# Optimization experiments

Measured on AMD Instinct MI355X. Metric: run time of the kernel, lower is better.

The kernel has to match this reference:

```python
import jax, jax.numpy as jnp
import numpy as np

B, N, DIM, H, DH = 2, 2048, 512, 8, 64
EPS = 1e-3  # eps added after relu feature map, per original


def setup_inputs() -> dict:
    key = jax.random.key(0)
    k0, k1, k2, k3, k4 = jax.random.split(key, 5)
    s_in = 1.0 / np.sqrt(DIM)
    s_out = 1.0 / np.sqrt(H * DH)
    return {
        "x": jax.random.normal(k0, (B, N, DIM), jnp.float32),
        "Wq": jax.random.normal(k1, (DIM, H * DH), jnp.float32) * s_in,
        "Wk": jax.random.normal(k2, (DIM, H * DH), jnp.float32) * s_in,
        "Wv": jax.random.normal(k3, (DIM, H * DH), jnp.float32) * s_in,
        "Wo": jax.random.normal(k4, (H * DH, DIM), jnp.float32) * s_out,
        "bo": jnp.zeros((DIM,), jnp.float32),
    }


def causal_linear_attn(q, k, v, eps=EPS):
    # bucket_size == 1 path of the original causal_linear_attn (blindspot_size=1):
    # relu feature map + eps, running cumsums of k and of the outer product k v^T.
    q = jax.nn.relu(q) + eps
    k = jax.nn.relu(k) + eps
    k_cum = jnp.cumsum(k, axis=2)                                  # [b,h,n,d]
    ctx = jnp.cumsum(k[..., :, None] * v[..., None, :], axis=2)    # [b,h,n,d,e]
    d_inv = 1.0 / jnp.einsum('bhnd,bhnd->bhn', q, k_cum)           # [b,h,n]
    return jnp.einsum('bhnd,bhnde,bhn->bhne', q, ctx, d_inv)       # [b,h,n,e]


def reference(x, Wq, Wk, Wv, Wo, bo):
    b, n, _ = x.shape
    split = lambda t: t.reshape(b, n, H, DH).transpose(0, 2, 1, 3)  # [b,h,n,dh]
    q = split(x @ Wq)
    k = split(x @ Wk)
    v = split(x @ Wv)
    out = causal_linear_attn(q, k, v)
    out = out.transpose(0, 2, 1, 3).reshape(b, n, H * DH)
    return out @ Wo + bo
```

## Files before the change

### kernel.cpp

```cpp
#include <hip/hip_runtime.h>

constexpr int kB   = 2;
constexpr int kN   = 2048;
constexpr int kDIM = 512;
constexpr int kH   = 8;
constexpr int kDH  = 64;
constexpr int kBH  = kB * kH;
constexpr int NROWS = kB * kN;
constexpr int CHUNK = 64;
constexpr int NCH   = kN / CHUNK;
constexpr int CBSTRIDE = kDH * kDH + kDH;
constexpr float kEPS = 1e-3f;

typedef _Float16 f16x8 __attribute__((ext_vector_type(8)));
typedef _Float16 f16x4 __attribute__((ext_vector_type(4)));
typedef float    floatx4 __attribute__((ext_vector_type(4)));

__device__ __forceinline__ void async_copy16(void* lds, const void* g) {
    __builtin_amdgcn_global_load_lds(
        (const __attribute__((address_space(1))) void*)g,
        (__attribute__((address_space(3))) void*)lds,
        16, 0, 0);
}

__global__ __launch_bounds__(256)
void prep_kernel(const float* __restrict__ Wq, const float* __restrict__ Wk,
                 const float* __restrict__ Wv, const float* __restrict__ Wo,
                 _Float16* __restrict__ WT, _Float16* __restrict__ WoT)
{
    __shared__ float tile[32][33];
    const int z = blockIdx.z;
    const float* src = (z == 0) ? Wq : (z == 1) ? Wk : (z == 2) ? Wv : Wo;
    _Float16* dst = (z < 3) ? (WT + (size_t)z * 512 * 512) : WoT;
    const int r0 = blockIdx.y * 32, c0 = blockIdx.x * 32;
    const int tr = threadIdx.x >> 5, tc = threadIdx.x & 31;
    #pragma unroll
    for (int i = 0; i < 4; ++i)
        tile[tr + 8 * i][tc] = src[(size_t)(r0 + tr + 8 * i) * 512 + c0 + tc];
    __syncthreads();
    #pragma unroll
    for (int i = 0; i < 4; ++i)
        dst[(size_t)(c0 + tr + 8 * i) * 512 + r0 + tc] = (_Float16)tile[tc][tr + 8 * i];
}

__global__ __launch_bounds__(256)
void qkv_gemm_kernel(const float* __restrict__ Af32,
                     const _Float16* __restrict__ BT,
                     _Float16* __restrict__ qh,
                     _Float16* __restrict__ khb,
                     _Float16* __restrict__ kTh,
                     _Float16* __restrict__ vTh)
{
    constexpr int K = 512;
    __shared__ _Float16 As[128 * 64];
    __shared__ _Float16 Bs[128 * 64];

    const int t = threadIdx.x;
    const int l = t & 63;
    const int w = t >> 6;
    const int wm = w >> 1, wn = w & 1;
    const int m0 = blockIdx.y * 128;
    const int n0 = blockIdx.x * 128;

    const int r15 = l & 15, kq = l >> 4, sw = r15 & 7;

    floatx4 acc[4][4];
    #pragma unroll
    for (int mi = 0; mi < 4; ++mi)
        #pragma unroll
        for (int ni = 0; ni < 4; ++ni)
            acc[mi][ni] = (floatx4){0.f, 0.f, 0.f, 0.f};

    const int srow  = t >> 3;
    const int sslot = t & 7;

    const char* Bbase = (const char*)(BT + (size_t)n0 * K);
    char* AsB = (char*)As;
    char* BsB = (char*)Bs;

    const char* ArdB = (const char*)As + (wm * 64 + r15) * 128;
    const char* BrdB = (const char*)Bs + (wn * 64 + r15) * 128;
    const int sw0 = ((kq ^ sw) << 4);
    const int sw1 = (((4 + kq) ^ sw) << 4);

    for (int k0 = 0; k0 < K; k0 += 64) {
        #pragma unroll
        for (int i = 0; i < 4; ++i) {
            const int row = i * 32 + srow;
            const int gsl = sslot ^ (row & 7);
            async_copy16(BsB + row * 128 + sslot * 16,
                         Bbase + (size_t)row * (K * 2) + k0 * 2 + gsl * 16);
        }
        #pragma unroll
        for (int i = 0; i < 4; ++i) {
            const int s = i * 256 + t;
            const int row = s >> 3, sl = s & 7;
            const float* xp = Af32 + (size_t)(m0 + row) * K + k0 + sl * 8;
            const float4 a0 = *(const float4*)(xp);
            const float4 a1 = *(const float4*)(xp + 4);
            f16x8 v;
            v[0] = (_Float16)a0.x; v[1] = (_Float16)a0.y;
            v[2] = (_Float16)a0.z; v[3] = (_Float16)a0.w;
            v[4] = (_Float16)a1.x; v[5] = (_Float16)a1.y;
            v[6] = (_Float16)a1.z; v[7] = (_Float16)a1.w;
            *(f16x8*)(AsB + row * 128 + ((sl ^ (row & 7)) << 4)) = v;
        }
        __syncthreads();

        f16x8 af[4][2], bf[4][2];
        #pragma unroll
        for (int i = 0; i < 4; ++i) {
            af[i][0] = *(const f16x8*)(ArdB + i * 2048 + sw0);
            af[i][1] = *(const f16x8*)(ArdB + i * 2048 + sw1);
            bf[i][0] = *(const f16x8*)(BrdB + i * 2048 + sw0);
            bf[i][1] = *(const f16x8*)(BrdB + i * 2048 + sw1);
        }
        #pragma unroll
        for (int kk = 0; kk < 2; ++kk)
            #pragma unroll
            for (int mi = 0; mi < 4; ++mi)
                #pragma unroll
                for (int ni = 0; ni < 4; ++ni)
                    acc[mi][ni] = __builtin_amdgcn_mfma_f32_16x16x32_f16(
                        af[mi][kk], bf[ni][kk], acc[mi][ni], 0, 0, 0);
        __syncthreads();
    }

    #pragma unroll
    for (int ni = 0; ni < 4; ++ni) {
        const int col = n0 + wn * 64 + ni * 16 + r15;
        const int which = col >> 9;
        const int h = (col >> 6) & 7, e = col & 63;
        #pragma unroll
        for (int mi = 0; mi < 4; ++mi) {
            const int row0 = m0 + wm * 64 + mi * 16 + kq * 4;
            const int b = row0 >> 11, nn = row0 & 2047;
            const int bh = b * 8 + h;
            float vv[4];
            #pragma unroll
            for (int r = 0; r < 4; ++r) {
                float v = acc[mi][ni][r];
                if (which < 2) v = fmaxf(v, 0.f) + kEPS;
                vv[r] = v;
            }
            if (which == 0) {
                #pragma unroll
                for (int r = 0; r < 4; ++r)
                    qh[((size_t)bh * kN + nn + r) * 64 + e] = (_Float16)vv[r];
            } else if (which == 1) {
                #pragma unroll
                for (int r = 0; r < 4; ++r)
                    khb[((size_t)bh * kN + nn + r) * 64 + e] = (_Float16)vv[r];
                f16x4 t4;
                t4[0] = (_Float16)vv[0]; t4[1] = (_Float16)vv[1];
                t4[2] = (_Float16)vv[2]; t4[3] = (_Float16)vv[3];
                *(f16x4*)(kTh + ((size_t)bh * 64 + e) * kN + nn) = t4;
            } else {
                f16x4 t4;
                t4[0] = (_Float16)vv[0]; t4[1] = (_Float16)vv[1];
                t4[2] = (_Float16)vv[2]; t4[3] = (_Float16)vv[3];
                *(f16x4*)(vTh + ((size_t)bh * 64 + e) * kN + nn) = t4;
            }
        }
    }
}

__global__ __launch_bounds__(256)
void chunk_sum_kernel(const _Float16* __restrict__ kTh, const _Float16* __restrict__ vTh,
                      float* __restrict__ cbuf)
{
    const int ch = blockIdx.x, bh = blockIdx.y;
    const int t = threadIdx.x, l = t & 63, w = t >> 6;
    const int r15 = l & 15, kq = l >> 4;

    const _Float16* vbase = vTh + (size_t)bh * 64 * kN + ch * 64;
    const _Float16* kbase = kTh + (size_t)bh * 64 * kN + ch * 64;

    f16x8 av[2], bk[4][2];
    #pragma unroll
    for (int kk = 0; kk < 2; ++kk) {
        av[kk] = *(const f16x8*)(vbase + (size_t)(w * 16 + r15) * kN + kk * 32 + kq * 8);
        #pragma unroll
        for (int ni = 0; ni < 4; ++ni)
            bk[ni][kk] = *(const f16x8*)(kbase + (size_t)(ni * 16 + r15) * kN + kk * 32 + kq * 8);
    }
    floatx4 acc[4];
    #pragma unroll
    for (int ni = 0; ni < 4; ++ni) acc[ni] = (floatx4){0.f, 0.f, 0.f, 0.f};
    #pragma unroll
    for (int kk = 0; kk < 2; ++kk)
        #pragma unroll
        for (int ni = 0; ni < 4; ++ni)
            acc[ni] = __builtin_amdgcn_mfma_f32_16x16x32_f16(av[kk], bk[ni][kk], acc[ni], 0, 0, 0);

    float* out = cbuf + ((size_t)bh * NCH + ch) * CBSTRIDE;
    #pragma unroll
    for (int ni = 0; ni < 4; ++ni)
        #pragma unroll
        for (int r = 0; r < 4; ++r)
            out[(size_t)(w * 16 + kq * 4 + r) * 64 + ni * 16 + r15] = acc[ni][r];

    if (t < 64) {
        const _Float16* kp = kbase + (size_t)t * kN;
        float z = 0.f;
        #pragma unroll
        for (int j = 0; j < 8; ++j) {
            f16x8 v8 = *(const f16x8*)(kp + j * 8);
            #pragma unroll
            for (int u = 0; u < 8; ++u) z += (float)v8[u];
        }
        out[4096 + t] = z;
    }
}

__global__ __launch_bounds__(256)
void prefix_kernel(const float* __restrict__ cbuf, _Float16* __restrict__ spre16,
                   float* __restrict__ zpre)
{
    const int bh = blockIdx.y;
    const int i = blockIdx.x * 256 + threadIdx.x;
    if (i >= CBSTRIDE) return;
    const float* src = cbuf + (size_t)bh * NCH * CBSTRIDE + i;
    _Float16* dst = spre16 + (size_t)bh * NCH * CBSTRIDE + i;
    float* zp = zpre + (size_t)bh * NCH * 64;
    const bool isz = (i >= 4096);
    float vals[NCH];
    #pragma unroll
    for (int c = 0; c < NCH; ++c) vals[c] = src[(size_t)c * CBSTRIDE];
    float a = 0.f;
    #pragma unroll
    for (int c = 0; c < NCH; ++c) {
        dst[(size_t)c * CBSTRIDE] = (_Float16)a;
        if (isz) zp[c * 64 + (i - 4096)] = a;
        a += vals[c];
    }
}

__global__ __launch_bounds__(256)
void chunk_out_kernel(const _Float16* __restrict__ qh, const _Float16* __restrict__ khb,
                      const _Float16* __restrict__ vTh, const _Float16* __restrict__ spre16,
                      const float* __restrict__ zpre, _Float16* __restrict__ attnh)
{
    const int ch = blockIdx.x, bh = blockIdx.y;
    const int t = threadIdx.x, l = t & 63, w = t >> 6;
    const int r15 = l & 15, kq = l >> 4;

    __shared__ _Float16 Plds[64 * 64];
    __shared__ float denp[64];
    __shared__ float denf[64];

    const size_t rowbase = (size_t)bh * kN + ch * 64;

    f16x8 aq[2], bk[4][2];
    #pragma unroll
    for (int kk = 0; kk < 2; ++kk) {
        aq[kk] = *(const f16x8*)(qh + (rowbase + w * 16 + r15) * 64 + kk * 32 + kq * 8);
        #pragma unroll
        for (int ni = 0; ni < 4; ++ni)
            bk[ni][kk] = *(const f16x8*)(khb + (rowbase + ni * 16 + r15) * 64 + kk * 32 + kq * 8);
    }
    floatx4 sacc[4];
    #pragma unroll
    for (int ni = 0; ni < 4; ++ni) sacc[ni] = (floatx4){0.f, 0.f, 0.f, 0.f};
    #pragma unroll
    for (int kk = 0; kk < 2; ++kk)
        #pragma unroll
        for (int ni = 0; ni < 4; ++ni)
            sacc[ni] = __builtin_amdgcn_mfma_f32_16x16x32_f16(aq[kk], bk[ni][kk], sacc[ni], 0, 0, 0);

    const int qrow = w * 16 + kq * 4;
    float psum[4] = {0.f, 0.f, 0.f, 0.f};
    #pragma unroll
    for (int ni = 0; ni < 4; ++ni) {
        const int m = ni * 16 + r15;
        #pragma unroll
        for (int r = 0; r < 4; ++r) {
            const int row = qrow + r;
            const float v = (m <= row) ? sacc[ni][r] : 0.f;
            psum[r] += v;
            const int byte = row * 128 + ((((unsigned)m >> 3) ^ (row & 7)) << 4) + (m & 7) * 2;
            *(_Float16*)((char*)Plds + byte) = (_Float16)v;
        }
    }
    #pragma unroll
    for (int r = 0; r < 4; ++r) {
        float p = psum[r];
        p += __shfl_xor(p, 1, 16);
        p += __shfl_xor(p, 2, 16);
        p += __shfl_xor(p, 4, 16);
        p += __shfl_xor(p, 8, 16);
        if (r15 == 0) denp[qrow + r] = p;
    }
    __syncthreads();

    if (t < 64) {
        const _Float16* qp = qh + (rowbase + t) * 64;
        const float* zp = zpre + ((size_t)bh * NCH + ch) * 64;
        float s = denp[t];
        #pragma unroll
        for (int j = 0; j < 8; ++j) {
            f16x8 q8 = *(const f16x8*)(qp + j * 8);
            #pragma unroll
            for (int u = 0; u < 8; ++u) s += (float)q8[u] * zp[j * 8 + u];
        }
        denf[t] = 1.0f / s;
    }

    f16x8 ap[2], bv[4][2], bs[4][2];
    #pragma unroll
    for (int km = 0; km < 2; ++km)
        ap[km] = *(const f16x8*)((char*)Plds + (w * 16 + r15) * 128 +
                                 (((km * 4 + kq) ^ (r15 & 7)) << 4));
    #pragma unroll
    for (int ni = 0; ni < 4; ++ni) {
        #pragma unroll
        for (int km = 0; km < 2; ++km)
            bv[ni][km] = *(const f16x8*)(vTh + ((size_t)bh * 64 + ni * 16 + r15) * kN +
                                         ch * 64 + km * 32 + kq * 8);
    }
    const _Float16* sp = spre16 + ((size_t)bh * NCH + ch) * CBSTRIDE;
    #pragma unroll
    for (int ni = 0; ni < 4; ++ni)
        #pragma unroll
        for (int kd = 0; kd < 2; ++kd)
            bs[ni][kd] = *(const f16x8*)(sp + (size_t)(ni * 16 + r15) * 64 + kd * 32 + kq * 8);

    floatx4 oacc[4];
    #pragma unroll
    for (int ni = 0; ni < 4; ++ni) oacc[ni] = (floatx4){0.f, 0.f, 0.f, 0.f};
    #pragma unroll
    for (int km = 0; km < 2; ++km)
        #pragma unroll
        for (int ni = 0; ni < 4; ++ni)
            oacc[ni] = __builtin_amdgcn_mfma_f32_16x16x32_f16(ap[km], bv[ni][km], oacc[ni], 0, 0, 0);
    #pragma unroll
    for (int kd = 0; kd < 2; ++kd)
        #pragma unroll
        for (int ni = 0; ni < 4; ++ni)
            oacc[ni] = __builtin_amdgcn_mfma_f32_16x16x32_f16(aq[kd], bs[ni][kd], oacc[ni], 0, 0, 0);
    __syncthreads();

    const int b = bh >> 3, h = bh & 7;
    #pragma unroll
    for (int ni = 0; ni < 4; ++ni) {
        const int e = ni * 16 + r15;
        #pragma unroll
        for (int r = 0; r < 4; ++r) {
            const int qn = qrow + r;
            const float ov = oacc[ni][r] * denf[qn];
            attnh[((size_t)(b * kN + ch * 64 + qn)) * 512 + h * 64 + e] = (_Float16)ov;
        }
    }
}

__global__ __launch_bounds__(256)
void out_gemm_kernel(const _Float16* __restrict__ A,
                     const _Float16* __restrict__ BT,
                     const float* __restrict__ bo,
                     float* __restrict__ outf)
{
    constexpr int K = 512;
    __shared__ _Float16 As[128 * 64];
    __shared__ _Float16 Bs[128 * 64];

    const int t = threadIdx.x;
    const int l = t & 63;
    const int w = t >> 6;
    const int wm = w >> 1, wn = w & 1;
    const int m0 = blockIdx.y * 128;
    const int n0 = blockIdx.x * 128;

    const int r15 = l & 15, kq = l >> 4, sw = r15 & 7;

    floatx4 acc[4][4];
    #pragma unroll
    for (int mi = 0; mi < 4; ++mi)
        #pragma unroll
        for (int ni = 0; ni < 4; ++ni)
            acc[mi][ni] = (floatx4){0.f, 0.f, 0.f, 0.f};

    const int srow  = t >> 3;
    const int sslot = t & 7;

    const char* Abase = (const char*)(A + (size_t)m0 * K);
    const char* Bbase = (const char*)(BT + (size_t)n0 * K);
    char* AsB = (char*)As;
    char* BsB = (char*)Bs;

    const char* ArdB = (const char*)As + (wm * 64 + r15) * 128;
    const char* BrdB = (const char*)Bs + (wn * 64 + r15) * 128;
    const int sw0 = ((kq ^ sw) << 4);
    const int sw1 = (((4 + kq) ^ sw) << 4);

    for (int k0 = 0; k0 < K; k0 += 64) {
        #pragma unroll
        for (int i = 0; i < 4; ++i) {
            const int row = i * 32 + srow;
            const int gsl = sslot ^ (row & 7);
            async_copy16(AsB + row * 128 + sslot * 16,
                         Abase + (size_t)row * (K * 2) + k0 * 2 + gsl * 16);
            async_copy16(BsB + row * 128 + sslot * 16,
                         Bbase + (size_t)row * (K * 2) + k0 * 2 + gsl * 16);
        }
        __syncthreads();

        f16x8 af[4][2], bf[4][2];
        #pragma unroll
        for (int i = 0; i < 4; ++i) {
            af[i][0] = *(const f16x8*)(ArdB + i * 2048 + sw0);
            af[i][1] = *(const f16x8*)(ArdB + i * 2048 + sw1);
            bf[i][0] = *(const f16x8*)(BrdB + i * 2048 + sw0);
            bf[i][1] = *(const f16x8*)(BrdB + i * 2048 + sw1);
        }
        #pragma unroll
        for (int kk = 0; kk < 2; ++kk)
            #pragma unroll
            for (int mi = 0; mi < 4; ++mi)
                #pragma unroll
                for (int ni = 0; ni < 4; ++ni)
                    acc[mi][ni] = __builtin_amdgcn_mfma_f32_16x16x32_f16(
                        af[mi][kk], bf[ni][kk], acc[mi][ni], 0, 0, 0);
        __syncthreads();
    }

    #pragma unroll
    for (int ni = 0; ni < 4; ++ni) {
        const int col = n0 + wn * 64 + ni * 16 + r15;
        const float bias = bo[col];
        #pragma unroll
        for (int mi = 0; mi < 4; ++mi) {
            const int row = m0 + wm * 64 + mi * 16 + kq * 4;
            #pragma unroll
            for (int r = 0; r < 4; ++r)
                outf[(size_t)(row + r) * 512 + col] = acc[mi][ni][r] + bias;
        }
    }
}

extern "C" void kernel_launch(void* const* d_in, const int* in_sizes, int n_in,
                              void* d_out, int out_size, void* d_ws, size_t ws_size,
                              hipStream_t stream)
{
    const float* x  = (const float*)d_in[0];
    const float* Wq = (const float*)d_in[1];
    const float* Wk = (const float*)d_in[2];
    const float* Wv = (const float*)d_in[3];
    const float* Wo = (const float*)d_in[4];
    const float* bo = (const float*)d_in[5];
    float* out = (float*)d_out;

    char* ws = (char*)d_ws;
    _Float16* qh     = (_Float16*)(ws + 0);
    _Float16* khb    = (_Float16*)(ws + 4194304);
    _Float16* kTh    = (_Float16*)(ws + 8388608);
    _Float16* vTh    = (_Float16*)(ws + 12582912);
    float*    cbuf   = (float*)(ws + 16777216);
    _Float16* spre16 = (_Float16*)(ws + 25296896);
    float*    zpre   = (float*)(ws + 29556736);
    _Float16* WT     = (_Float16*)(ws + 29687808);
    _Float16* WoT    = (_Float16*)(ws + 31260672);
    _Float16* attnh  = (_Float16*)(ws + 31784960);

    prep_kernel<<<dim3(16, 16, 4), 256, 0, stream>>>(Wq, Wk, Wv, Wo, WT, WoT);
    qkv_gemm_kernel<<<dim3(12, NROWS / 128), 256, 0, stream>>>(
        x, WT, qh, khb, kTh, vTh);
    chunk_sum_kernel<<<dim3(NCH, kBH), 256, 0, stream>>>(kTh, vTh, cbuf);
    prefix_kernel<<<dim3(17, kBH), 256, 0, stream>>>(cbuf, spre16, zpre);
    chunk_out_kernel<<<dim3(NCH, kBH), 256, 0, stream>>>(
        qh, khb, vTh, spre16, zpre, attnh);
    out_gemm_kernel<<<dim3(4, NROWS / 128), 256, 0, stream>>>(
        attnh, WoT, bo, out);
}
```

Measured before the change: 60.60 us.

## Pre-convert x to fp16 and widen QKV GEMM tile with async A loads

The prep kernel gains extra blocks that convert the fp32 input x into an fp16 copy in workspace. The QKV GEMM then streams A with the same async global-to-LDS copies already used for B, instead of loading fp32 through registers and converting inline. The GEMM block tile widens from 128x128 to 128x256 with 512 threads, which halves how often each A tile is re-read. The costs are an extra full pass over x, more LDS per block, and only 192 GEMM blocks, which may leave compute units idle.

```diff
diff --git a/kernel.cpp b/kernel.cpp
--- a/kernel.cpp
+++ b/kernel.cpp
@@ -26,10 +26,22 @@
 __global__ __launch_bounds__(256)
 void prep_kernel(const float* __restrict__ Wq, const float* __restrict__ Wk,
                  const float* __restrict__ Wv, const float* __restrict__ Wo,
-                 _Float16* __restrict__ WT, _Float16* __restrict__ WoT)
-{
+                 const float* __restrict__ x,
+                 _Float16* __restrict__ WT, _Float16* __restrict__ WoT,
+                 _Float16* __restrict__ xh)
+{
+    const int z = blockIdx.z;
+    if (z >= 4) {
+        const size_t base = (((size_t)(z - 4) * 256 + blockIdx.y * 16 + blockIdx.x) * 256 +
+                             threadIdx.x) * 4;
+        const float4 a = *(const float4*)(x + base);
+        f16x4 o;
+        o[0] = (_Float16)a.x; o[1] = (_Float16)a.y;
+        o[2] = (_Float16)a.z; o[3] = (_Float16)a.w;
+        *(f16x4*)(xh + base) = o;
+        return;
+    }
     __shared__ float tile[32][33];
-    const int z = blockIdx.z;
     const float* src = (z == 0) ? Wq : (z == 1) ? Wk : (z == 2) ? Wv : Wo;
     _Float16* dst = (z < 3) ? (WT + (size_t)z * 512 * 512) : WoT;
     const int r0 = blockIdx.y * 32, c0 = blockIdx.x * 32;
@@ -43,8 +55,8 @@
         dst[(size_t)(c0 + tr + 8 * i) * 512 + r0 + tc] = (_Float16)tile[tc][tr + 8 * i];
 }
 
-__global__ __launch_bounds__(256)
-void qkv_gemm_kernel(const float* __restrict__ Af32,
+__global__ __launch_bounds__(512)
+void qkv_gemm_kernel(const _Float16* __restrict__ A,
                      const _Float16* __restrict__ BT,
                      _Float16* __restrict__ qh,
                      _Float16* __restrict__ khb,
@@ -53,14 +65,14 @@
 {
     constexpr int K = 512;
     __shared__ _Float16 As[128 * 64];
-    __shared__ _Float16 Bs[128 * 64];
+    __shared__ _Float16 Bs[256 * 64];
 
     const int t = threadIdx.x;
     const int l = t & 63;
     const int w = t >> 6;
-    const int wm = w >> 1, wn = w & 1;
+    const int wm = w >> 2, wn = w & 3;
     const int m0 = blockIdx.y * 128;
-    const int n0 = blockIdx.x * 128;
+    const int n0 = blockIdx.x * 256;
 
     const int r15 = l & 15, kq = l >> 4, sw = r15 & 7;
 
@@ -71,9 +83,7 @@
         for (int ni = 0; ni < 4; ++ni)
             acc[mi][ni] = (floatx4){0.f, 0.f, 0.f, 0.f};
 
-    const int srow  = t >> 3;
-    const int sslot = t & 7;
-
+    const char* Abase = (const char*)(A + (size_t)m0 * K);
     const char* Bbase = (const char*)(BT + (size_t)n0 * K);
     char* AsB = (char*)As;
     char* BsB = (char*)Bs;
@@ -85,25 +95,20 @@
 
     for (int k0 = 0; k0 < K; k0 += 64) {
         #pragma unroll
+        for (int i = 0; i < 2; ++i) {
+            const int s = i * 512 + t;
+            const int row = s >> 3, sl = s & 7;
+            const int gsl = sl ^ (row & 7);
+            async_copy16(AsB + row * 128 + sl * 16,
+                         Abase + (size_t)row * (K * 2) + k0 * 2 + gsl * 16);
+        }
+        #pragma unroll
         for (int i = 0; i < 4; ++i) {
-            const int row = i * 32 + srow;
-            const int gsl = sslot ^ (row & 7);
-            async_copy16(BsB + row * 128 + sslot * 16,
+            const int s = i * 512 + t;
+            const int row = s >> 3, sl = s & 7;
+            const int gsl = sl ^ (row & 7);
+            async_copy16(BsB + row * 128 + sl * 16,
                          Bbase + (size_t)row * (K * 2) + k0 * 2 + gsl * 16);
-        }
-        #pragma unroll
-        for (int i = 0; i < 4; ++i) {
-            const int s = i * 256 + t;
-            const int row = s >> 3, sl = s & 7;
-            const float* xp = Af32 + (size_t)(m0 + row) * K + k0 + sl * 8;
-            const float4 a0 = *(const float4*)(xp);
-            const float4 a1 = *(const float4*)(xp + 4);
-            f16x8 v;
-            v[0] = (_Float16)a0.x; v[1] = (_Float16)a0.y;
-            v[2] = (_Float16)a0.z; v[3] = (_Float16)a0.w;
-            v[4] = (_Float16)a1.x; v[5] = (_Float16)a1.y;
-            v[6] = (_Float16)a1.z; v[7] = (_Float16)a1.w;
-            *(f16x8*)(AsB + row * 128 + ((sl ^ (row & 7)) << 4)) = v;
         }
         __syncthreads();
 
@@ -460,10 +465,11 @@
     _Float16* WT     = (_Float16*)(ws + 29687808);
     _Float16* WoT    = (_Float16*)(ws + 31260672);
     _Float16* attnh  = (_Float16*)(ws + 31784960);
-
-    prep_kernel<<<dim3(16, 16, 4), 256, 0, stream>>>(Wq, Wk, Wv, Wo, WT, WoT);
-    qkv_gemm_kernel<<<dim3(12, NROWS / 128), 256, 0, stream>>>(
-        x, WT, qh, khb, kTh, vTh);
+    _Float16* xh     = (_Float16*)(ws + 35979264);
+
+    prep_kernel<<<dim3(16, 16, 12), 256, 0, stream>>>(Wq, Wk, Wv, Wo, x, WT, WoT, xh);
+    qkv_gemm_kernel<<<dim3(6, NROWS / 128), 512, 0, stream>>>(
+        xh, WT, qh, khb, kTh, vTh);
     chunk_sum_kernel<<<dim3(NCH, kBH), 256, 0, stream>>>(kTh, vTh, cbuf);
     prefix_kernel<<<dim3(17, kBH), 256, 0, stream>>>(cbuf, spre16, zpre);
     chunk_out_kernel<<<dim3(NCH, kBH), 256, 0, stream>>>(
```

Measured after the change: 58.07 us. 1.04x faster.
